# Optimization experiments

Hardware: AMD Instinct MI355X
Metric: run time of the kernel (lower is better)

The kernel has to match this reference:

```python
import jax, jax.numpy as jnp
import numpy as np

DIM = 128
N_CONV = 4
N_GRAPHS = 256
EPS = 1e-5


def _layernorm(h, g, b):
    m = jnp.mean(h, axis=-1, keepdims=True)
    v = jnp.mean((h - m) ** 2, axis=-1, keepdims=True)
    return g * (h - m) / jnp.sqrt(v + 1e-5) + b


def _gated_gcn(x, ei, e, Wsrc, bsrc, Wdst, bdst, We, be, nxg, nxb, neg, neb):
    # x: [N, D] node feats, ei: [2, E], e: [E, D] edge feats
    n = x.shape[0]
    i, j = ei[0], ei[1]
    sig = jax.nn.sigmoid(e)                                   # [E, D]
    e_sum = jax.ops.segment_sum(sig, i, num_segments=n)       # [N, D]
    e_gated = sig / (e_sum[i] + EPS)                          # [E, D]
    msg = e_gated * (x[j] @ Wdst + bdst)                      # [E, D]
    agg = jax.ops.segment_sum(msg, i, num_segments=n)         # [N, D]
    out = x @ Wsrc + bsrc + agg
    out = x + jax.nn.silu(_layernorm(out, nxg, nxb))
    z = jnp.concatenate([x[i], x[j], e], axis=-1)             # [E, 3D]
    e_new = e + jax.nn.silu(_layernorm(z @ We + be, neg, neb))
    return out, e_new


def setup_inputs() -> dict:
    key = jax.random.key(0)
    ks = iter(jax.random.split(key, 64))
    d = DIM

    def rn(shape, s=0.05):
        return (jax.random.normal(next(ks), shape, dtype=jnp.float32) * s)

    inp = {}
    inp["x"] = jax.random.normal(next(ks), (20000, 92), dtype=jnp.float32)
    inp["edge_attr"] = jax.random.normal(next(ks), (320000, 50), dtype=jnp.float32)
    inp["edge_attr_line"] = jax.random.normal(next(ks), (600000, 40), dtype=jnp.float32)
    inp["edge_index"] = jax.random.randint(next(ks), (2, 320000), 0, 20000, dtype=jnp.int64)
    inp["edge_index_line"] = jax.random.randint(next(ks), (2, 600000), 0, 320000, dtype=jnp.int64)
    inp["batch"] = jnp.sort(jax.random.randint(next(ks), (20000,), 0, N_GRAPHS, dtype=jnp.int64))

    inp["pre1_W"] = rn((92, d)); inp["pre1_b"] = jnp.zeros((d,), jnp.float32)
    inp["pre2_W"] = rn((50, d)); inp["pre2_b"] = jnp.zeros((d,), jnp.float32)
    inp["pre3_W"] = rn((40, d)); inp["pre3_b"] = jnp.zeros((d,), jnp.float32)

    for pfx in ("line", "atom"):
        inp[pfx + "_Wsrc"] = rn((N_CONV, d, d)); inp[pfx + "_bsrc"] = jnp.zeros((N_CONV, d), jnp.float32)
        inp[pfx + "_Wdst"] = rn((N_CONV, d, d)); inp[pfx + "_bdst"] = jnp.zeros((N_CONV, d), jnp.float32)
        inp[pfx + "_We"] = rn((N_CONV, 3 * d, d)); inp[pfx + "_be"] = jnp.zeros((N_CONV, d), jnp.float32)
        inp[pfx + "_nxg"] = jnp.ones((N_CONV, d), jnp.float32); inp[pfx + "_nxb"] = jnp.zeros((N_CONV, d), jnp.float32)
        inp[pfx + "_neg"] = jnp.ones((N_CONV, d), jnp.float32); inp[pfx + "_neb"] = jnp.zeros((N_CONV, d), jnp.float32)

    inp["bn_g"] = jnp.ones((d,), jnp.float32); inp["bn_b"] = jnp.zeros((d,), jnp.float32)
    inp["post_W"] = rn((d, d)); inp["post_b"] = jnp.zeros((d,), jnp.float32)
    inp["out_W"] = rn((d, 1)); inp["out_b"] = jnp.zeros((1,), jnp.float32)
    return inp


def reference(x, edge_attr, edge_attr_line,
              pre1_W, pre1_b, pre2_W, pre2_b, pre3_W, pre3_b,
              line_Wsrc, line_bsrc, line_Wdst, line_bdst, line_We, line_be,
              line_nxg, line_nxb, line_neg, line_neb,
              atom_Wsrc, atom_bsrc, atom_Wdst, atom_bdst, atom_We, atom_be,
              atom_nxg, atom_nxb, atom_neg, atom_neb,
              bn_g, bn_b, post_W, post_b, out_W, out_b,
              edge_index, edge_index_line, batch):
    act = jax.nn.silu
    # pre-FC (single layer each)
    h_node = act(x @ pre1_W + pre1_b)              # [N, D]
    h_edge = act(edge_attr @ pre2_W + pre2_b)      # [E, D]
    h_line = act(edge_attr_line @ pre3_W + pre3_b) # [E_line, D]

    for l in range(N_CONV):
        # line graph conv: nodes = atom edges, edges = line-graph edges
        h_edge, h_line = _gated_gcn(h_edge, edge_index_line, h_line,
                                    line_Wsrc[l], line_bsrc[l], line_Wdst[l], line_bdst[l],
                                    line_We[l], line_be[l],
                                    line_nxg[l], line_nxb[l], line_neg[l], line_neb[l])
        # atom graph conv
        h_node, h_edge = _gated_gcn(h_node, edge_index, h_edge,
                                    atom_Wsrc[l], atom_bsrc[l], atom_Wdst[l], atom_bdst[l],
                                    atom_We[l], atom_be[l],
                                    atom_nxg[l], atom_nxb[l], atom_neg[l], atom_neb[l])
        # dropout_rate = 0 -> identity

    # BatchNorm1d (batch statistics over nodes)
    m = jnp.mean(h_node, axis=0)
    v = jnp.mean((h_node - m) ** 2, axis=0)
    out = bn_g * (h_node - m) / jnp.sqrt(v + 1e-5) + bn_b
    out = act(out)
    out = act(out @ post_W + post_b)

    # global mean pool over crystals
    sums = jax.ops.segment_sum(out, batch, num_segments=N_GRAPHS)
    cnts = jax.ops.segment_sum(jnp.ones((out.shape[0],), out.dtype), batch, num_segments=N_GRAPHS)
    pooled = sums / jnp.maximum(cnts, 1.0)[:, None]
    return (pooled @ out_W + out_b).reshape(-1)    # [N_GRAPHS]
```

## Files before the change

### kernel.cpp

```cpp
#include <hip/hip_runtime.h>

#define NCONV_DEF 4
#define SCH 1024

typedef unsigned short u16;
typedef __attribute__((ext_vector_type(8))) short s8v;
typedef __attribute__((ext_vector_type(4))) float f4v;
typedef __attribute__((ext_vector_type(8))) unsigned short u16x8;

__device__ __forceinline__ float sigm_f(float x){ return 1.f/(1.f+__expf(-x)); }
__device__ __forceinline__ float silu_f(float x){ return x/(1.f+__expf(-x)); }
__device__ __forceinline__ float b2f(u16 h){ union{unsigned u; float f;} v; v.u=(unsigned)h<<16; return v.f; }
__device__ __forceinline__ u16 f2b(float f){ union{float f; unsigned u;} v; v.f=f; unsigned r=v.u+0x7fffu+((v.u>>16)&1u); return (u16)(r>>16); }
__device__ __forceinline__ float ldAv(const float* p, size_t i){ return p[i]; }
__device__ __forceinline__ float ldAv(const u16* p, size_t i){ return b2f(p[i]); }

#define EPS_ 136

__global__ __launch_bounds__(256) void zero_f_k(float* p, long n){
    long i=(long)blockIdx.x*256+threadIdx.x, st=(long)gridDim.x*256;
    for(;i<n;i+=st) p[i]=0.f;
}
__global__ __launch_bounds__(256) void zero_i_k(int* p, long n){
    long i=(long)blockIdx.x*256+threadIdx.x, st=(long)gridDim.x*256;
    for(;i<n;i+=st) p[i]=0;
}
__global__ void diag_k(float* out, int n, float v){
    int i=blockIdx.x*256+threadIdx.x; if(i<n) out[i]=v;
}
__global__ void probe_k(const int* ei, const int* eil, const int* batch, int nb, int* flag){
    if(threadIdx.x||blockIdx.x) return;
    int a=2,b=2,c=2;
    for(int k=0;k<64;k++){ if(ei[2*k+1]!=0) a=1; if(eil[2*k+1]!=0) b=1; }
    int base=nb-128;
    for(int k=0;k<64;k++){ if(batch[base+2*k+1]!=0) c=1; }
    flag[0]=a; flag[1]=b; flag[2]=c;
}

__global__ __launch_bounds__(256)
void hist_k(const int* __restrict__ idx, const int* __restrict__ iflag, int fi,
            int* __restrict__ cnt, int Ne, int Nn){
    int e=blockIdx.x*256+threadIdx.x; if(e>=Ne) return;
    int st=iflag[fi];
    int i=idx[(size_t)e*st]; i=i<0?0:(i>=Nn?Nn-1:i);
    atomicAdd(&cnt[i],1);
}
__global__ __launch_bounds__(256)
void scan1_k(const int* cnt, int* tot, int n){
    __shared__ int sh[256];
    int base=blockIdx.x*SCH, s=0;
    for(int t=threadIdx.x;t<SCH;t+=256){ int i=base+t; s+=(i<n)?cnt[i]:0; }
    sh[threadIdx.x]=s; __syncthreads();
    for(int o=128;o;o>>=1){ if(threadIdx.x<o) sh[threadIdx.x]+=sh[threadIdx.x+o]; __syncthreads(); }
    if(threadIdx.x==0) tot[blockIdx.x]=sh[0];
}
__global__ void scan2_k(int* tot, int nb){
    if(threadIdx.x==0&&blockIdx.x==0){ int acc=0; for(int i=0;i<nb;i++){int v=tot[i]; tot[i]=acc; acc+=v;} }
}
__global__ __launch_bounds__(256)
void scan3_k(const int* cnt, const int* tot, int* off, int n, int total){
    __shared__ int sh[256];
    int b=blockIdx.x, t4=b*SCH+threadIdx.x*4;
    int v0=(t4+0<n)?cnt[t4+0]:0, v1=(t4+1<n)?cnt[t4+1]:0;
    int v2=(t4+2<n)?cnt[t4+2]:0, v3=(t4+3<n)?cnt[t4+3]:0;
    int ls=v0+v1+v2+v3;
    sh[threadIdx.x]=ls; __syncthreads();
    for(int o=1;o<256;o<<=1){
        int val=(threadIdx.x>=o)?sh[threadIdx.x-o]:0; __syncthreads();
        sh[threadIdx.x]+=val; __syncthreads();
    }
    int excl=sh[threadIdx.x]-ls+tot[b];
    if(t4+0<n) off[t4+0]=excl;
    if(t4+1<n) off[t4+1]=excl+v0;
    if(t4+2<n) off[t4+2]=excl+v0+v1;
    if(t4+3<n) off[t4+3]=excl+v0+v1+v2;
    if(b==(int)gridDim.x-1&&threadIdx.x==255) off[n]=total;
}
__global__ __launch_bounds__(256)
void fill_k(const int* __restrict__ idx, const int* __restrict__ iflag, int fi, long joff,
            const int* __restrict__ off, int* __restrict__ cur,
            int* __restrict__ list, int* __restrict__ jlist, int Ne, int Nn){
    int e=blockIdx.x*256+threadIdx.x; if(e>=Ne) return;
    int st=iflag[fi];
    int i=idx[(size_t)e*st]; i=i<0?0:(i>=Nn?Nn-1:i);
    int j=idx[((size_t)joff+e)*st]; j=j<0?0:(j>=Nn?Nn-1:j);
    int pos=off[i]+atomicAdd(&cur[i],1);
    list[pos]=e; jlist[pos]=j;
}

__global__ __launch_bounds__(256)
void pack_w_k(const float* __restrict__ W, u16* __restrict__ Wp, int K, int Kp){
    int i=blockIdx.x*256+threadIdx.x;
    if(i>=128*Kp) return;
    int n=i/Kp, k=i-n*Kp;
    Wp[i] = (k<K) ? f2b(W[(size_t)k*128+n]) : (u16)0;
}

template<typename TA, int ACT>
__global__ __launch_bounds__(256)
void gemm_k(const TA* __restrict__ A, int lda, int M, int K, int Kp,
            const u16* __restrict__ Wp, const float* __restrict__ bias,
            u16* __restrict__ C)
{
    __shared__ __align__(16) u16 As[64*72];
    __shared__ __align__(16) u16 Bs[128*72];
    const int tid=threadIdx.x, row0=blockIdx.x*64;
    const int w=tid>>6, l=tid&63, lr=l&15, kg=l>>4;
    f4v zz={0.f,0.f,0.f,0.f};
    f4v acc[8];
#pragma unroll
    for(int i=0;i<8;++i) acc[i]=zz;

    for(int kt=0;kt<Kp;kt+=64){
        {
            int r=tid>>2, c0=(tid&3)*16;
            int gr=row0+r;
            bool vec=false;
            if constexpr (sizeof(TA)==2) vec=((K&63)==0);
            if(vec){
                const u16* src=(const u16*)(const void*)A+(size_t)gr*lda+kt+c0;
                u16x8 v0={0,0,0,0,0,0,0,0}, v1={0,0,0,0,0,0,0,0};
                if(gr<M){ v0=*(const u16x8*)src; v1=*(const u16x8*)(src+8); }
                *(u16x8*)&As[r*72+c0]=v0;
                *(u16x8*)&As[r*72+c0+8]=v1;
            } else {
                for(int c=c0;c<c0+16;++c){
                    int k=kt+c;
                    float v=(gr<M&&k<K)?ldAv(A,(size_t)gr*lda+k):0.f;
                    As[r*72+c]=f2b(v);
                }
            }
        }
        {
            int n=tid>>1, k0=(tid&1)*32;
            const u16* src=Wp+(size_t)n*Kp+kt+k0;
            *(u16x8*)&Bs[n*72+k0]   =*(const u16x8*)(src);
            *(u16x8*)&Bs[n*72+k0+8] =*(const u16x8*)(src+8);
            *(u16x8*)&Bs[n*72+k0+16]=*(const u16x8*)(src+16);
            *(u16x8*)&Bs[n*72+k0+24]=*(const u16x8*)(src+24);
        }
        __syncthreads();
        const int arow=w*16+lr;
#pragma unroll
        for(int kk=0;kk<64;kk+=32){
            s8v a=*(const s8v*)&As[arow*72+kk+kg*8];
#pragma unroll
            for(int ct=0;ct<8;++ct){
                s8v bfr=*(const s8v*)&Bs[(ct*16+lr)*72+kk+kg*8];
                acc[ct]=__builtin_amdgcn_mfma_f32_16x16x32_bf16(a,bfr,acc[ct],0,0,0);
            }
        }
        __syncthreads();
    }
    u16* ep=Bs;
#pragma unroll
    for(int ct=0;ct<8;++ct){
        int col=ct*16+lr;
        float bv=bias?bias[col]:0.f;
#pragma unroll
        for(int reg=0;reg<4;++reg){
            float v=acc[ct][reg]+bv;
            if(ACT) v=silu_f(v);
            ep[(w*16+kg*4+reg)*EPS_+col]=f2b(v);
        }
    }
    __syncthreads();
    {
        int ar=tid>>2, gr=row0+ar;
        if(gr<M){
            u16* crow=C+(size_t)gr*128+(tid&3)*32;
            const u16* hrow=&ep[ar*EPS_+(tid&3)*32];
#pragma unroll
            for(int c4=0;c4<4;++c4)
                *(u16x8*)(crow+c4*8)=*(const u16x8*)(hrow+c4*8);
        }
    }
}

__global__ __launch_bounds__(256)
void gemmz_k(u16* __restrict__ X, int M,
             const u16* __restrict__ Wp, const float* __restrict__ bias,
             const u16* __restrict__ U,
             const float* __restrict__ g, const float* __restrict__ b)
{
    __shared__ __align__(16) u16 As[2][64*68];
    __shared__ __align__(16) u16 Bs[128*136];
    const int tid=threadIdx.x, row0=blockIdx.x*64;
    const int w=tid>>6, l=tid&63, lr=l&15, kg=l>>4;
    u16* ep=&As[0][0];
    const int ar=tid>>2, gr=row0+ar;
    {
        u16x8 z8={0,0,0,0,0,0,0,0};
        u16x8 u0=z8,u1=z8,u2=z8,u3=z8;
        if(gr<M){
            const u16* ur=U+(size_t)gr*128+(tid&3)*32;
            u0=*(const u16x8*)(ur); u1=*(const u16x8*)(ur+8);
            u2=*(const u16x8*)(ur+16); u3=*(const u16x8*)(ur+24);
        }
        u16* d=&ep[ar*EPS_+(tid&3)*32];
        *(u16x8*)(d)=u0; *(u16x8*)(d+8)=u1; *(u16x8*)(d+16)=u2; *(u16x8*)(d+24)=u3;
    }
    __syncthreads();
    f4v acc[8];
#pragma unroll
    for(int ct=0;ct<8;++ct){
        int col=ct*16+lr;
        float bv=bias[col];
#pragma unroll
        for(int reg=0;reg<4;++reg)
            acc[ct][reg]=b2f(ep[(w*16+kg*4+reg)*EPS_+col])+bv;
    }
    __syncthreads();

    {
        int c0=(tid&3)*16;
        const u16* src=X+(size_t)gr*128;
        u16x8 z8={0,0,0,0,0,0,0,0};
        u16x8 v0=z8,v1=z8,v2=z8,v3=z8;
        if(gr<M){
            v0=*(const u16x8*)(src+c0);    v1=*(const u16x8*)(src+c0+8);
            v2=*(const u16x8*)(src+64+c0); v3=*(const u16x8*)(src+64+c0+8);
        }
        *(u16x8*)&As[0][ar*68+c0]=v0;  *(u16x8*)&As[0][ar*68+c0+8]=v1;
        *(u16x8*)&As[1][ar*68+c0]=v2;  *(u16x8*)&As[1][ar*68+c0+8]=v3;
        int bn=tid>>1, bk=(tid&1)*64;
        const u16* wsrc=Wp+(size_t)bn*128+bk;
#pragma unroll
        for(int q=0;q<8;++q)
            *(u16x8*)&Bs[bn*136+bk+q*8]=*(const u16x8*)(wsrc+q*8);
    }
    __syncthreads();
    const int arow=w*16+lr;
#pragma unroll
    for(int kt=0;kt<2;++kt){
#pragma unroll
        for(int kk=0;kk<64;kk+=32){
            s8v a=*(const s8v*)&As[kt][arow*68+kk+kg*8];
#pragma unroll
            for(int ct=0;ct<8;++ct){
                s8v bfr=*(const s8v*)&Bs[(ct*16+lr)*136+kt*64+kk+kg*8];
                acc[ct]=__builtin_amdgcn_mfma_f32_16x16x32_bf16(a,bfr,acc[ct],0,0,0);
            }
        }
    }
    float sum[4]={0.f,0.f,0.f,0.f}, sq[4]={0.f,0.f,0.f,0.f};
#pragma unroll
    for(int ct=0;ct<8;++ct)
#pragma unroll
        for(int reg=0;reg<4;++reg){
            float v=acc[ct][reg];
            sum[reg]+=v; sq[reg]+=v*v;
        }
#pragma unroll
    for(int m=1;m<16;m<<=1)
#pragma unroll
        for(int reg=0;reg<4;++reg){
            sum[reg]+=__shfl_xor(sum[reg],m,64);
            sq[reg] +=__shfl_xor(sq[reg], m,64);
        }
    float mean[4], rstd[4];
#pragma unroll
    for(int reg=0;reg<4;++reg){
        mean[reg]=sum[reg]*(1.f/128.f);
        float var=sq[reg]*(1.f/128.f)-mean[reg]*mean[reg];
        rstd[reg]=rsqrtf(var+1e-5f);
    }
    __syncthreads();
#pragma unroll
    for(int ct=0;ct<8;++ct){
        int col=ct*16+lr;
        float gv=g[col], bv=b[col];
#pragma unroll
        for(int reg=0;reg<4;++reg){
            float h=gv*(acc[ct][reg]-mean[reg])*rstd[reg]+bv;
            ep[(w*16+kg*4+reg)*EPS_+col]=f2b(silu_f(h));
        }
    }
    if(gr<M){
        u16* xrow=X+(size_t)gr*128+(tid&3)*32;
        const u16* hrow=&ep[ar*EPS_+(tid&3)*32];
#pragma unroll
        for(int c4=0;c4<4;++c4){
            u16x8 xv=*(const u16x8*)(xrow+c4*8);
            u16x8 hv=*(const u16x8*)(hrow+c4*8);
            u16x8 ov;
#pragma unroll
            for(int j=0;j<8;++j) ov[j]=f2b(b2f(xv[j])+b2f(hv[j]));
            *(u16x8*)(xrow+c4*8)=ov;
        }
    }
}

template<int FIN, int HASPREV>
__global__ __launch_bounds__(256)
void gather_k(const u16* __restrict__ e, const u16* __restrict__ P1,
              u16* __restrict__ U,
              const int* __restrict__ off, const int* __restrict__ list,
              const int* __restrict__ jlist,
              int Nn, int c0, int c1)
{
    int wid=threadIdx.x>>6, lane=threadIdx.x&63;
    int h=lane>>5, sl=lane&31;
    int n=blockIdx.x*8+wid*2+h;
    int beg=0,end=0;
    if(n<Nn){ beg=off[n]; end=off[n+1]; }
    const int d4=sl*4;
    uint2 uprev; uprev.x=0; uprev.y=0;
    if(FIN&&HASPREV&&n<Nn) uprev=*(const uint2*)(U+(size_t)n*128+d4);

    float es[4]={0.f,0.f,0.f,0.f}, a[4]={0.f,0.f,0.f,0.f};
    int k=beg;
    uint2 ev_n, pv_n; ev_n.x=ev_n.y=0; pv_n.x=pv_n.y=0;
    bool in_n=false;
    if(k<end){
        int eid=list[k], j=jlist[k];
        in_n=(j>=c0)&&(j<c1);
        if(FIN||in_n) ev_n=*(const uint2*)(e+(size_t)eid*128+d4);
        if(in_n)      pv_n=*(const uint2*)(P1+(size_t)(j-c0)*128+d4);
    }
    while(k<end){
        uint2 ev=ev_n, pv=pv_n; bool in=in_n;
        int kn=k+1;
        if(kn<end){
            int eid=list[kn], j=jlist[kn];
            in_n=(j>=c0)&&(j<c1);
            ev_n.x=ev_n.y=0; pv_n.x=pv_n.y=0;
            if(FIN||in_n) ev_n=*(const uint2*)(e+(size_t)eid*128+d4);
            if(in_n)      pv_n=*(const uint2*)(P1+(size_t)(j-c0)*128+d4);
        }
        float s0=sigm_f(b2f((u16)(ev.x&0xffff)));
        float s1=sigm_f(b2f((u16)(ev.x>>16)));
        float s2=sigm_f(b2f((u16)(ev.y&0xffff)));
        float s3=sigm_f(b2f((u16)(ev.y>>16)));
        if(FIN){ es[0]+=s0; es[1]+=s1; es[2]+=s2; es[3]+=s3; }
        if(in){
            a[0]+=s0*b2f((u16)(pv.x&0xffff));
            a[1]+=s1*b2f((u16)(pv.x>>16));
            a[2]+=s2*b2f((u16)(pv.y&0xffff));
            a[3]+=s3*b2f((u16)(pv.y>>16));
        }
        k=kn;
    }
    if(n>=Nn) return;
    uint2* up=(uint2*)(U+(size_t)n*128+d4);
    uint2 o;
    if(!FIN){
        o.x=((unsigned)f2b(a[0]))|((unsigned)f2b(a[1])<<16);
        o.y=((unsigned)f2b(a[2]))|((unsigned)f2b(a[3])<<16);
    } else {
        if(HASPREV){
            a[0]+=b2f((u16)(uprev.x&0xffff));
            a[1]+=b2f((u16)(uprev.x>>16));
            a[2]+=b2f((u16)(uprev.y&0xffff));
            a[3]+=b2f((u16)(uprev.y>>16));
        }
        float r0=1.f/(es[0]+1e-5f), r1=1.f/(es[1]+1e-5f);
        float r2=1.f/(es[2]+1e-5f), r3=1.f/(es[3]+1e-5f);
        o.x=((unsigned)f2b(a[0]*r0))|((unsigned)f2b(a[1]*r1)<<16);
        o.y=((unsigned)f2b(a[2]*r2))|((unsigned)f2b(a[3]*r3)<<16);
    }
    *up=o;
}

__global__ __launch_bounds__(512)
void edgez_k(u16* __restrict__ e, const u16* __restrict__ x,
             const int* __restrict__ idx, long joff,
             const int* __restrict__ iflag, int fi,
             const u16* __restrict__ Wep, const float* __restrict__ be,
             const float* __restrict__ g, const float* __restrict__ b,
             int Ne, int Nn)
{
    __shared__ __align__(16) u16 As[2][128*68];
    __shared__ __align__(16) u16 Bs[2][128*68];
    __shared__ int rid[256];
    const int tid=threadIdx.x, row0=blockIdx.x*128;
    const int w=tid>>6, l=tid&63, lr=l&15, kg=l>>4;
    int st=iflag[fi];
    if(tid<256){
        int r=tid&127, eid=row0+r; if(eid>=Ne) eid=Ne-1;
        long elem=(tid<128)?(long)eid:(joff+eid);
        int v=idx[(size_t)elem*st]; v=v<0?0:(v>=Nn?Nn-1:v);
        rid[tid]=v;
    }
    __syncthreads();
    const int ar=tid>>2, ac=(tid&3)*16;
    const int bn=tid>>2, bk=(tid&3)*16;
    int eidA=row0+ar; if(eidA>=Ne) eidA=Ne-1;
    const u16* aptr0=x+(size_t)rid[ar]*128;
    const u16* aptr1=x+(size_t)rid[128+ar]*128;
    const u16* aptr2=e+(size_t)eidA*128;

    f4v zz={0.f,0.f,0.f,0.f};
    f4v acc[8];
#pragma unroll
    for(int i=0;i<8;++i) acc[i]=zz;

    u16x8 a0,a1,b0,b1;
    u16x8 er0,er1,er2,er3;
    {
        const u16* src=aptr0+ac;
        a0=*(const u16x8*)src; a1=*(const u16x8*)(src+8);
        const u16* wsrc=Wep+(size_t)bn*384+bk;
        b0=*(const u16x8*)wsrc; b1=*(const u16x8*)(wsrc+8);
    }
#pragma unroll
    for(int s=0;s<6;++s){
        const int buf=s&1;
        *(u16x8*)&As[buf][ar*68+ac]  =a0;
        *(u16x8*)&As[buf][ar*68+ac+8]=a1;
        *(u16x8*)&Bs[buf][bn*68+bk]  =b0;
        *(u16x8*)&Bs[buf][bn*68+bk+8]=b1;
        if(s<5){
            const int sn=s+1, sec=sn>>1, half=sn&1;
            const u16* src=(sec==0?aptr0:(sec==1?aptr1:aptr2))+half*64+ac;
            a0=*(const u16x8*)src; a1=*(const u16x8*)(src+8);
            if(sec==2){ if(half==0){ er0=a0; er1=a1; } else { er2=a0; er3=a1; } }
            const u16* wsrc=Wep+(size_t)bn*384+sn*64+bk;
            b0=*(const u16x8*)wsrc; b1=*(const u16x8*)(wsrc+8);
        }
        __syncthreads();
        __builtin_amdgcn_s_setprio(1);
        const int arow=w*16+lr;
#pragma unroll
        for(int kk=0;kk<64;kk+=32){
            s8v a=*(const s8v*)&As[buf][arow*68+kk+kg*8];
#pragma unroll
            for(int ct=0;ct<8;++ct){
                s8v bfr=*(const s8v*)&Bs[buf][(ct*16+lr)*68+kk+kg*8];
                acc[ct]=__builtin_amdgcn_mfma_f32_16x16x32_bf16(a,bfr,acc[ct],0,0,0);
            }
        }
        __builtin_amdgcn_s_setprio(0);
    }
    float sum[4]={0.f,0.f,0.f,0.f}, sq[4]={0.f,0.f,0.f,0.f};
#pragma unroll
    for(int ct=0;ct<8;++ct){
        float bev=be[ct*16+lr];
#pragma unroll
        for(int reg=0;reg<4;++reg){
            float v=acc[ct][reg]+bev;
            acc[ct][reg]=v;
            sum[reg]+=v; sq[reg]+=v*v;
        }
    }
#pragma unroll
    for(int m=1;m<16;m<<=1){
#pragma unroll
        for(int reg=0;reg<4;++reg){
            sum[reg]+=__shfl_xor(sum[reg],m,64);
            sq[reg] +=__shfl_xor(sq[reg], m,64);
        }
    }
    float mean[4], rstd[4];
#pragma unroll
    for(int reg=0;reg<4;++reg){
        mean[reg]=sum[reg]*(1.f/128.f);
        float var=sq[reg]*(1.f/128.f)-mean[reg]*mean[reg];
        rstd[reg]=rsqrtf(var+1e-5f);
    }
    __syncthreads();
    u16* ep=&Bs[0][0];
#pragma unroll
    for(int ct=0;ct<8;++ct){
        int col=ct*16+lr;
        float gv=g[col], bv=b[col];
#pragma unroll
        for(int reg=0;reg<4;++reg){
            float hh=gv*(acc[ct][reg]-mean[reg])*rstd[reg]+bv;
            ep[(w*16+kg*4+reg)*EPS_+col]=f2b(silu_f(hh));
        }
    }
    {
        int eid=row0+ar;
        if(eid<Ne){
            u16* erow=e+(size_t)eid*128;
            const u16* hr=&ep[ar*EPS_];
            u16x8 h0=*(const u16x8*)(hr+ac),    h1=*(const u16x8*)(hr+ac+8);
            u16x8 h2=*(const u16x8*)(hr+64+ac), h3=*(const u16x8*)(hr+64+ac+8);
            u16x8 o0,o1,o2,o3;
#pragma unroll
            for(int j=0;j<8;++j){
                o0[j]=f2b(b2f(er0[j])+b2f(h0[j]));
                o1[j]=f2b(b2f(er1[j])+b2f(h1[j]));
                o2[j]=f2b(b2f(er2[j])+b2f(h2[j]));
                o3[j]=f2b(b2f(er3[j])+b2f(h3[j]));
            }
            *(u16x8*)(erow+ac)=o0;    *(u16x8*)(erow+ac+8)=o1;
            *(u16x8*)(erow+64+ac)=o2; *(u16x8*)(erow+64+ac+8)=o3;
        }
    }
}

__global__ __launch_bounds__(256)
void bn_stats_k(const u16* __restrict__ h, float* __restrict__ st, int N){
    int t=blockIdx.x*256+threadIdx.x;
    int d=t&127, r0=t>>7, rstride=(gridDim.x*256)>>7;
    float s=0.f,q=0.f;
    for(int r=r0;r<N;r+=rstride){ float v=b2f(h[(size_t)r*128+d]); s+=v; q+=v*v; }
    atomicAdd(&st[d],s); atomicAdd(&st[128+d],q);
}
__global__ __launch_bounds__(256)
void bn_apply_k(u16* __restrict__ h, const float* __restrict__ st,
                const float* __restrict__ g, const float* __restrict__ b, int N){
    int t=blockIdx.x*256+threadIdx.x;
    if(t>=N*128) return;
    int d=t&127;
    float inv=1.f/(float)N;
    float m=st[d]*inv, var=st[128+d]*inv-m*m;
    float v=g[d]*(b2f(h[t])-m)*rsqrtf(var+1e-5f)+b[d];
    h[t]=f2b(silu_f(v));
}
__global__ __launch_bounds__(256)
void pool_k(const u16* __restrict__ o, const int* __restrict__ batch,
            const int* __restrict__ iflag,
            float* __restrict__ pooled, float* __restrict__ cnt, int N, int NG){
    int st=iflag[2];
    int wid=threadIdx.x>>6, lane=threadIdx.x&63;
    int n=blockIdx.x*4+wid; if(n>=N) return;
    int gi=batch[(size_t)n*st]; gi=gi<0?0:(gi>=NG?NG-1:gi);
    atomicAdd(&pooled[(size_t)gi*128+lane],    b2f(o[(size_t)n*128+lane]));
    atomicAdd(&pooled[(size_t)gi*128+64+lane], b2f(o[(size_t)n*128+64+lane]));
    if(lane==0) atomicAdd(&cnt[gi],1.f);
}
__global__ void final_k(const float* __restrict__ pooled, const float* __restrict__ cnt,
                        const float* __restrict__ oW, const float* __restrict__ ob,
                        float* __restrict__ out){
    int gi=blockIdx.x, lane=threadIdx.x;
    float v=pooled[(size_t)gi*128+lane]*oW[lane]
           +pooled[(size_t)gi*128+64+lane]*oW[64+lane];
    for(int m=32;m;m>>=1) v+=__shfl_xor(v,m,64);
    if(lane==0) out[gi]=v/fmaxf(cnt[gi],1.f)+ob[0];
}

template<typename TA>
static inline void gemm(hipStream_t s, const TA* A, int lda, int M, int K, int Kp,
                        const u16* Wp, const float* bias, u16* C, int act){
    dim3 grid((M+63)/64);
    if(act) gemm_k<TA,1><<<grid,256,0,s>>>(A,lda,M,K,Kp,Wp,bias,C);
    else    gemm_k<TA,0><<<grid,256,0,s>>>(A,lda,M,K,Kp,Wp,bias,C);
}

static inline void build_csr(hipStream_t s, const int* idx, int fi, long joff, const int* iflag,
                             int Ne, int Nn, int* off, int* cur, int* list, int* jlist, int* tot){
    int nb=(Nn+SCH-1)/SCH;
    zero_i_k<<<256,256,0,s>>>(cur,Nn);
    hist_k<<<(Ne+255)/256,256,0,s>>>(idx,iflag,fi,cur,Ne,Nn);
    scan1_k<<<nb,256,0,s>>>(cur,tot,Nn);
    scan2_k<<<1,1,0,s>>>(tot,nb);
    scan3_k<<<nb,256,0,s>>>(cur,tot,off,Nn,Ne);
    zero_i_k<<<256,256,0,s>>>(cur,Nn);
    fill_k<<<(Ne+255)/256,256,0,s>>>(idx,iflag,fi,joff,off,cur,list,jlist,Ne,Nn);
}

static inline void pack_w(hipStream_t s, const float* W, u16* Wp, int K, int Kp){
    pack_w_k<<<(128*Kp+255)/256,256,0,s>>>(W,Wp,K,Kp);
}

extern "C" void kernel_launch(void* const* d_in, const int* in_sizes, int n_in,
                              void* d_out, int out_size, void* d_ws, size_t ws_size,
                              hipStream_t stream)
{
    const float* x_in =(const float*)d_in[0];
    const float* ea   =(const float*)d_in[1];
    const float* eal  =(const float*)d_in[2];
    const int*   ei   =(const int*)d_in[3];
    const int*   eil  =(const int*)d_in[4];
    const int*   batch=(const int*)d_in[5];
    const float* pre1W=(const float*)d_in[6];  const float* pre1b=(const float*)d_in[7];
    const float* pre2W=(const float*)d_in[8];  const float* pre2b=(const float*)d_in[9];
    const float* pre3W=(const float*)d_in[10]; const float* pre3b=(const float*)d_in[11];
    const float* lWsrc=(const float*)d_in[12]; const float* lbsrc=(const float*)d_in[13];
    const float* lWdst=(const float*)d_in[14]; const float* lbdst=(const float*)d_in[15];
    const float* lWe  =(const float*)d_in[16]; const float* lbe  =(const float*)d_in[17];
    const float* lnxg =(const float*)d_in[18]; const float* lnxb =(const float*)d_in[19];
    const float* lneg =(const float*)d_in[20]; const float* lneb =(const float*)d_in[21];
    const float* aWsrc=(const float*)d_in[22]; const float* absrc=(const float*)d_in[23];
    const float* aWdst=(const float*)d_in[24]; const float* abdst=(const float*)d_in[25];
    const float* aWe  =(const float*)d_in[26]; const float* abe  =(const float*)d_in[27];
    const float* anxg =(const float*)d_in[28]; const float* anxb =(const float*)d_in[29];
    const float* aneg =(const float*)d_in[30]; const float* aneb =(const float*)d_in[31];
    const float* bng  =(const float*)d_in[32]; const float* bnb  =(const float*)d_in[33];
    const float* postW=(const float*)d_in[34]; const float* postb=(const float*)d_in[35];
    const float* outW =(const float*)d_in[36]; const float* outb =(const float*)d_in[37];
    (void)n_in;

    const int N =in_sizes[5];
    const int E =in_sizes[3]/2;
    const int EL=in_sizes[4]/2;
    const int NG=out_size;
    const int CH=(E+1)/2;

    char* base=(char*)d_ws;
    size_t off=0;
    auto alloc=[&](size_t bytes)->char*{
        char* p=base+off; off=(off+bytes+255)&~(size_t)255; return p;
    };
    u16* hN   =(u16*)alloc((size_t)N*128*2);
    u16* hE   =(u16*)alloc((size_t)E*128*2);
    u16* hL   =(u16*)alloc((size_t)EL*128*2);
    u16* U    =(u16*)alloc((size_t)E*128*2);
    u16* P1   =(u16*)alloc((size_t)CH*128*2);
    int* off_l=(int*)alloc((size_t)(E+1)*4);
    int* cur_l=(int*)alloc((size_t)E*4);
    int* list_l=(int*)alloc((size_t)EL*4);
    int* jlist_l=(int*)alloc((size_t)EL*4);
    int* off_a=(int*)alloc((size_t)(N+1)*4);
    int* cur_a=(int*)alloc((size_t)N*4);
    int* list_a=(int*)alloc((size_t)E*4);
    int* jlist_a=(int*)alloc((size_t)E*4);
    int* tot  =(int*)alloc(4096);
    int* iflag=(int*)alloc(64);
    float* stats =(float*)alloc(256*4);
    float* pooled=(float*)alloc((size_t)NG*128*4);
    float* cnt   =(float*)alloc((size_t)NG*4);
    u16* pre1p=(u16*)alloc(128*128*2);
    u16* pre2p=(u16*)alloc(128*64*2);
    u16* pre3p=(u16*)alloc(128*64*2);
    u16* postp=(u16*)alloc(128*128*2);
    u16 *lsrcp[4],*ldstp[4],*lWep[4],*asrcp[4],*adstp[4],*aWep[4];
    for(int i=0;i<4;i++){
        lsrcp[i]=(u16*)alloc(128*128*2);
        ldstp[i]=(u16*)alloc(128*128*2);
        lWep[i] =(u16*)alloc(128*384*2);
        asrcp[i]=(u16*)alloc(128*128*2);
        adstp[i]=(u16*)alloc(128*128*2);
        aWep[i] =(u16*)alloc(128*384*2);
    }
    if(off>ws_size){
        diag_k<<<(NG+255)/256,256,0,stream>>>((float*)d_out,NG,(float)(ws_size>>20)+0.25f);
        return;
    }

    probe_k<<<1,64,0,stream>>>(ei,eil,batch,N,iflag);
    build_csr(stream,eil,1,EL,iflag,EL,E,off_l,cur_l,list_l,jlist_l,tot);
    build_csr(stream,ei, 0,E, iflag,E, N,off_a,cur_a,list_a,jlist_a,tot);

    pack_w(stream,pre1W,pre1p,92,128);
    pack_w(stream,pre2W,pre2p,50,64);
    pack_w(stream,pre3W,pre3p,40,64);
    pack_w(stream,postW,postp,128,128);
    for(int i=0;i<4;i++){
        pack_w(stream,lWsrc+(size_t)i*128*128,lsrcp[i],128,128);
        pack_w(stream,lWdst+(size_t)i*128*128,ldstp[i],128,128);
        pack_w(stream,lWe  +(size_t)i*384*128,lWep[i],384,384);
        pack_w(stream,aWsrc+(size_t)i*128*128,asrcp[i],128,128);
        pack_w(stream,aWdst+(size_t)i*128*128,adstp[i],128,128);
        pack_w(stream,aWe  +(size_t)i*384*128,aWep[i],384,384);
    }

    gemm(stream,x_in,92,N, 92,128,pre1p,pre1b,hN,1);
    gemm(stream,ea,  50,E, 50, 64,pre2p,pre2b,hE,1);
    gemm(stream,eal, 40,EL,40, 64,pre3p,pre3b,hL,1);

    for(int l=0;l<NCONV_DEF;++l){
        {
            gemm(stream,hE,128,CH,128,128,ldstp[l],lbdst+l*128,P1,0);
            gather_k<0,0><<<(E+7)/8,256,0,stream>>>(hL,P1,U,off_l,list_l,jlist_l,E,0,CH);
            gemm(stream,hE+(size_t)CH*128,128,E-CH,128,128,ldstp[l],lbdst+l*128,P1,0);
            gather_k<1,1><<<(E+7)/8,256,0,stream>>>(hL,P1,U,off_l,list_l,jlist_l,E,CH,E);
            edgez_k<<<(EL+127)/128,512,0,stream>>>(hL,hE,eil,EL,iflag,1,
                                                   lWep[l],lbe+l*128,lneg+l*128,lneb+l*128,EL,E);
            gemmz_k<<<(E+63)/64,256,0,stream>>>(hE,E,lsrcp[l],lbsrc+l*128,U,
                                                lnxg+l*128,lnxb+l*128);
        }
        {
            gemm(stream,hN,128,N,128,128,adstp[l],abdst+l*128,P1,0);
            gather_k<1,0><<<(N+7)/8,256,0,stream>>>(hE,P1,U,off_a,list_a,jlist_a,N,0,N);
            edgez_k<<<(E+127)/128,512,0,stream>>>(hE,hN,ei,E,iflag,0,
                                                  aWep[l],abe+l*128,aneg+l*128,aneb+l*128,E,N);
            gemmz_k<<<(N+63)/64,256,0,stream>>>(hN,N,asrcp[l],absrc+l*128,U,
                                                anxg+l*128,anxb+l*128);
        }
    }

    zero_f_k<<<64,256,0,stream>>>(stats,256);
    zero_f_k<<<64,256,0,stream>>>(pooled,(long)NG*128);
    zero_f_k<<<1,256,0,stream>>>(cnt,NG);
    bn_stats_k<<<256,256,0,stream>>>(hN,stats,N);
    bn_apply_k<<<(N*128+255)/256,256,0,stream>>>(hN,stats,bng,bnb,N);

    gemm(stream,hN,128,N,128,128,postp,postb,P1,1);

    pool_k<<<(N+3)/4,256,0,stream>>>(P1,batch,iflag,pooled,cnt,N,NG);
    final_k<<<NG,64,0,stream>>>(pooled,cnt,outW,outb,(float*)d_out);
}
```

Baseline: 3.109 ms.

## Halve edgez_k K-tile to shrink shared memory and raise occupancy

```diff
diff --git a/kernel.cpp b/kernel.cpp
--- a/kernel.cpp
+++ b/kernel.cpp
@@ -362,7 +362,7 @@
     *up=o;
 }
 
-__global__ __launch_bounds__(512)
+__global__ __launch_bounds__(512, 8)
 void edgez_k(u16* __restrict__ e, const u16* __restrict__ x,
              const int* __restrict__ idx, long joff,
              const int* __restrict__ iflag, int fi,
@@ -370,8 +370,7 @@
              const float* __restrict__ g, const float* __restrict__ b,
              int Ne, int Nn)
 {
-    __shared__ __align__(16) u16 As[2][128*68];
-    __shared__ __align__(16) u16 Bs[2][128*68];
+    __shared__ __align__(16) u16 smem[4*128*36];
     __shared__ int rid[256];
     const int tid=threadIdx.x, row0=blockIdx.x*128;
     const int w=tid>>6, l=tid&63, lr=l&15, kg=l>>4;
@@ -383,52 +382,45 @@
         rid[tid]=v;
     }
     __syncthreads();
-    const int ar=tid>>2, ac=(tid&3)*16;
-    const int bn=tid>>2, bk=(tid&3)*16;
+    const int ar=tid>>2, c8=(tid&3)*8;
     int eidA=row0+ar; if(eidA>=Ne) eidA=Ne-1;
     const u16* aptr0=x+(size_t)rid[ar]*128;
     const u16* aptr1=x+(size_t)rid[128+ar]*128;
     const u16* aptr2=e+(size_t)eidA*128;
+    u16* Asb[2]={smem,           smem+128*36};
+    u16* Bsb[2]={smem+2*128*36,  smem+3*128*36};
 
     f4v zz={0.f,0.f,0.f,0.f};
     f4v acc[8];
 #pragma unroll
     for(int i=0;i<8;++i) acc[i]=zz;
 
-    u16x8 a0,a1,b0,b1;
-    u16x8 er0,er1,er2,er3;
+    u16x8 a0,b0;
+    u16x8 er[4];
     {
-        const u16* src=aptr0+ac;
-        a0=*(const u16x8*)src; a1=*(const u16x8*)(src+8);
-        const u16* wsrc=Wep+(size_t)bn*384+bk;
-        b0=*(const u16x8*)wsrc; b1=*(const u16x8*)(wsrc+8);
-    }
-#pragma unroll
-    for(int s=0;s<6;++s){
+        a0=*(const u16x8*)(aptr0+c8);
+        b0=*(const u16x8*)(Wep+(size_t)ar*384+c8);
+    }
+#pragma unroll
+    for(int s=0;s<12;++s){
         const int buf=s&1;
-        *(u16x8*)&As[buf][ar*68+ac]  =a0;
-        *(u16x8*)&As[buf][ar*68+ac+8]=a1;
-        *(u16x8*)&Bs[buf][bn*68+bk]  =b0;
-        *(u16x8*)&Bs[buf][bn*68+bk+8]=b1;
-        if(s<5){
-            const int sn=s+1, sec=sn>>1, half=sn&1;
-            const u16* src=(sec==0?aptr0:(sec==1?aptr1:aptr2))+half*64+ac;
-            a0=*(const u16x8*)src; a1=*(const u16x8*)(src+8);
-            if(sec==2){ if(half==0){ er0=a0; er1=a1; } else { er2=a0; er3=a1; } }
-            const u16* wsrc=Wep+(size_t)bn*384+sn*64+bk;
-            b0=*(const u16x8*)wsrc; b1=*(const u16x8*)(wsrc+8);
+        *(u16x8*)&Asb[buf][ar*36+c8]=a0;
+        *(u16x8*)&Bsb[buf][ar*36+c8]=b0;
+        if(s<11){
+            const int sn=s+1, sec=sn>>2, soff=sn&3;
+            const u16* src=(sec==0?aptr0:(sec==1?aptr1:aptr2))+soff*32+c8;
+            a0=*(const u16x8*)src;
+            if(sec==2) er[soff]=a0;
+            b0=*(const u16x8*)(Wep+(size_t)ar*384+sn*32+c8);
         }
         __syncthreads();
         __builtin_amdgcn_s_setprio(1);
         const int arow=w*16+lr;
-#pragma unroll
-        for(int kk=0;kk<64;kk+=32){
-            s8v a=*(const s8v*)&As[buf][arow*68+kk+kg*8];
-#pragma unroll
-            for(int ct=0;ct<8;++ct){
-                s8v bfr=*(const s8v*)&Bs[buf][(ct*16+lr)*68+kk+kg*8];
-                acc[ct]=__builtin_amdgcn_mfma_f32_16x16x32_bf16(a,bfr,acc[ct],0,0,0);
-            }
+        s8v a=*(const s8v*)&Asb[buf][arow*36+kg*8];
+#pragma unroll
+        for(int ct=0;ct<8;++ct){
+            s8v bfr=*(const s8v*)&Bsb[buf][(ct*16+lr)*36+kg*8];
+            acc[ct]=__builtin_amdgcn_mfma_f32_16x16x32_bf16(a,bfr,acc[ct],0,0,0);
         }
         __builtin_amdgcn_s_setprio(0);
     }
@@ -459,7 +451,7 @@
         rstd[reg]=rsqrtf(var+1e-5f);
     }
     __syncthreads();
-    u16* ep=&Bs[0][0];
+    u16* ep=smem;
 #pragma unroll
     for(int ct=0;ct<8;++ct){
         int col=ct*16+lr;
@@ -475,18 +467,14 @@
         if(eid<Ne){
             u16* erow=e+(size_t)eid*128;
             const u16* hr=&ep[ar*EPS_];
-            u16x8 h0=*(const u16x8*)(hr+ac),    h1=*(const u16x8*)(hr+ac+8);
-            u16x8 h2=*(const u16x8*)(hr+64+ac), h3=*(const u16x8*)(hr+64+ac+8);
-            u16x8 o0,o1,o2,o3;
-#pragma unroll
-            for(int j=0;j<8;++j){
-                o0[j]=f2b(b2f(er0[j])+b2f(h0[j]));
-                o1[j]=f2b(b2f(er1[j])+b2f(h1[j]));
-                o2[j]=f2b(b2f(er2[j])+b2f(h2[j]));
-                o3[j]=f2b(b2f(er3[j])+b2f(h3[j]));
+#pragma unroll
+            for(int s4=0;s4<4;++s4){
+                u16x8 hv=*(const u16x8*)(hr+s4*32+c8);
+                u16x8 ov;
+#pragma unroll
+                for(int j=0;j<8;++j) ov[j]=f2b(b2f(er[s4][j])+b2f(hv[j]));
+                *(u16x8*)(erow+s4*32+c8)=ov;
             }
-            *(u16x8*)(erow+ac)=o0;    *(u16x8*)(erow+ac+8)=o1;
-            *(u16x8*)(erow+64+ac)=o2; *(u16x8*)(erow+64+ac+8)=o3;
         }
     }
 }
```

Measured after the change: 5.722 ms. 84.1% more time.

## Fuse final neighbor gather into node-update GEMM with ping-pong feature buffers

Applied to the files above, without the earlier changes.

```diff
diff --git a/kernel.cpp b/kernel.cpp
--- a/kernel.cpp
+++ b/kernel.cpp
@@ -178,126 +178,11 @@
 }
 
 __global__ __launch_bounds__(256)
-void gemmz_k(u16* __restrict__ X, int M,
-             const u16* __restrict__ Wp, const float* __restrict__ bias,
-             const u16* __restrict__ U,
-             const float* __restrict__ g, const float* __restrict__ b)
-{
-    __shared__ __align__(16) u16 As[2][64*68];
-    __shared__ __align__(16) u16 Bs[128*136];
-    const int tid=threadIdx.x, row0=blockIdx.x*64;
-    const int w=tid>>6, l=tid&63, lr=l&15, kg=l>>4;
-    u16* ep=&As[0][0];
-    const int ar=tid>>2, gr=row0+ar;
-    {
-        u16x8 z8={0,0,0,0,0,0,0,0};
-        u16x8 u0=z8,u1=z8,u2=z8,u3=z8;
-        if(gr<M){
-            const u16* ur=U+(size_t)gr*128+(tid&3)*32;
-            u0=*(const u16x8*)(ur); u1=*(const u16x8*)(ur+8);
-            u2=*(const u16x8*)(ur+16); u3=*(const u16x8*)(ur+24);
-        }
-        u16* d=&ep[ar*EPS_+(tid&3)*32];
-        *(u16x8*)(d)=u0; *(u16x8*)(d+8)=u1; *(u16x8*)(d+16)=u2; *(u16x8*)(d+24)=u3;
-    }
-    __syncthreads();
-    f4v acc[8];
-#pragma unroll
-    for(int ct=0;ct<8;++ct){
-        int col=ct*16+lr;
-        float bv=bias[col];
-#pragma unroll
-        for(int reg=0;reg<4;++reg)
-            acc[ct][reg]=b2f(ep[(w*16+kg*4+reg)*EPS_+col])+bv;
-    }
-    __syncthreads();
-
-    {
-        int c0=(tid&3)*16;
-        const u16* src=X+(size_t)gr*128;
-        u16x8 z8={0,0,0,0,0,0,0,0};
-        u16x8 v0=z8,v1=z8,v2=z8,v3=z8;
-        if(gr<M){
-            v0=*(const u16x8*)(src+c0);    v1=*(const u16x8*)(src+c0+8);
-            v2=*(const u16x8*)(src+64+c0); v3=*(const u16x8*)(src+64+c0+8);
-        }
-        *(u16x8*)&As[0][ar*68+c0]=v0;  *(u16x8*)&As[0][ar*68+c0+8]=v1;
-        *(u16x8*)&As[1][ar*68+c0]=v2;  *(u16x8*)&As[1][ar*68+c0+8]=v3;
-        int bn=tid>>1, bk=(tid&1)*64;
-        const u16* wsrc=Wp+(size_t)bn*128+bk;
-#pragma unroll
-        for(int q=0;q<8;++q)
-            *(u16x8*)&Bs[bn*136+bk+q*8]=*(const u16x8*)(wsrc+q*8);
-    }
-    __syncthreads();
-    const int arow=w*16+lr;
-#pragma unroll
-    for(int kt=0;kt<2;++kt){
-#pragma unroll
-        for(int kk=0;kk<64;kk+=32){
-            s8v a=*(const s8v*)&As[kt][arow*68+kk+kg*8];
-#pragma unroll
-            for(int ct=0;ct<8;++ct){
-                s8v bfr=*(const s8v*)&Bs[(ct*16+lr)*136+kt*64+kk+kg*8];
-                acc[ct]=__builtin_amdgcn_mfma_f32_16x16x32_bf16(a,bfr,acc[ct],0,0,0);
-            }
-        }
-    }
-    float sum[4]={0.f,0.f,0.f,0.f}, sq[4]={0.f,0.f,0.f,0.f};
-#pragma unroll
-    for(int ct=0;ct<8;++ct)
-#pragma unroll
-        for(int reg=0;reg<4;++reg){
-            float v=acc[ct][reg];
-            sum[reg]+=v; sq[reg]+=v*v;
-        }
-#pragma unroll
-    for(int m=1;m<16;m<<=1)
-#pragma unroll
-        for(int reg=0;reg<4;++reg){
-            sum[reg]+=__shfl_xor(sum[reg],m,64);
-            sq[reg] +=__shfl_xor(sq[reg], m,64);
-        }
-    float mean[4], rstd[4];
-#pragma unroll
-    for(int reg=0;reg<4;++reg){
-        mean[reg]=sum[reg]*(1.f/128.f);
-        float var=sq[reg]*(1.f/128.f)-mean[reg]*mean[reg];
-        rstd[reg]=rsqrtf(var+1e-5f);
-    }
-    __syncthreads();
-#pragma unroll
-    for(int ct=0;ct<8;++ct){
-        int col=ct*16+lr;
-        float gv=g[col], bv=b[col];
-#pragma unroll
-        for(int reg=0;reg<4;++reg){
-            float h=gv*(acc[ct][reg]-mean[reg])*rstd[reg]+bv;
-            ep[(w*16+kg*4+reg)*EPS_+col]=f2b(silu_f(h));
-        }
-    }
-    if(gr<M){
-        u16* xrow=X+(size_t)gr*128+(tid&3)*32;
-        const u16* hrow=&ep[ar*EPS_+(tid&3)*32];
-#pragma unroll
-        for(int c4=0;c4<4;++c4){
-            u16x8 xv=*(const u16x8*)(xrow+c4*8);
-            u16x8 hv=*(const u16x8*)(hrow+c4*8);
-            u16x8 ov;
-#pragma unroll
-            for(int j=0;j<8;++j) ov[j]=f2b(b2f(xv[j])+b2f(hv[j]));
-            *(u16x8*)(xrow+c4*8)=ov;
-        }
-    }
-}
-
-template<int FIN, int HASPREV>
-__global__ __launch_bounds__(256)
-void gather_k(const u16* __restrict__ e, const u16* __restrict__ P1,
-              u16* __restrict__ U,
-              const int* __restrict__ off, const int* __restrict__ list,
-              const int* __restrict__ jlist,
-              int Nn, int c0, int c1)
+void gatherp_k(const u16* __restrict__ e, const u16* __restrict__ P1,
+               u16* __restrict__ U,
+               const int* __restrict__ off, const int* __restrict__ list,
+               const int* __restrict__ jlist,
+               int Nn, int c0, int c1)
 {
     int wid=threadIdx.x>>6, lane=threadIdx.x&63;
     int h=lane>>5, sl=lane&31;
@@ -305,18 +190,17 @@
     int beg=0,end=0;
     if(n<Nn){ beg=off[n]; end=off[n+1]; }
     const int d4=sl*4;
-    uint2 uprev; uprev.x=0; uprev.y=0;
-    if(FIN&&HASPREV&&n<Nn) uprev=*(const uint2*)(U+(size_t)n*128+d4);
-
-    float es[4]={0.f,0.f,0.f,0.f}, a[4]={0.f,0.f,0.f,0.f};
+    float a[4]={0.f,0.f,0.f,0.f};
     int k=beg;
     uint2 ev_n, pv_n; ev_n.x=ev_n.y=0; pv_n.x=pv_n.y=0;
     bool in_n=false;
     if(k<end){
         int eid=list[k], j=jlist[k];
         in_n=(j>=c0)&&(j<c1);
-        if(FIN||in_n) ev_n=*(const uint2*)(e+(size_t)eid*128+d4);
-        if(in_n)      pv_n=*(const uint2*)(P1+(size_t)(j-c0)*128+d4);
+        if(in_n){
+            ev_n=*(const uint2*)(e+(size_t)eid*128+d4);
+            pv_n=*(const uint2*)(P1+(size_t)(j-c0)*128+d4);
+        }
     }
     while(k<end){
         uint2 ev=ev_n, pv=pv_n; bool in=in_n;
@@ -325,15 +209,16 @@
             int eid=list[kn], j=jlist[kn];
             in_n=(j>=c0)&&(j<c1);
             ev_n.x=ev_n.y=0; pv_n.x=pv_n.y=0;
-            if(FIN||in_n) ev_n=*(const uint2*)(e+(size_t)eid*128+d4);
-            if(in_n)      pv_n=*(const uint2*)(P1+(size_t)(j-c0)*128+d4);
-        }
-        float s0=sigm_f(b2f((u16)(ev.x&0xffff)));
-        float s1=sigm_f(b2f((u16)(ev.x>>16)));
-        float s2=sigm_f(b2f((u16)(ev.y&0xffff)));
-        float s3=sigm_f(b2f((u16)(ev.y>>16)));
-        if(FIN){ es[0]+=s0; es[1]+=s1; es[2]+=s2; es[3]+=s3; }
+            if(in_n){
+                ev_n=*(const uint2*)(e+(size_t)eid*128+d4);
+                pv_n=*(const uint2*)(P1+(size_t)(j-c0)*128+d4);
+            }
+        }
         if(in){
+            float s0=sigm_f(b2f((u16)(ev.x&0xffff)));
+            float s1=sigm_f(b2f((u16)(ev.x>>16)));
+            float s2=sigm_f(b2f((u16)(ev.y&0xffff)));
+            float s3=sigm_f(b2f((u16)(ev.y>>16)));
             a[0]+=s0*b2f((u16)(pv.x&0xffff));
             a[1]+=s1*b2f((u16)(pv.x>>16));
             a[2]+=s2*b2f((u16)(pv.y&0xffff));
@@ -342,24 +227,173 @@
         k=kn;
     }
     if(n>=Nn) return;
-    uint2* up=(uint2*)(U+(size_t)n*128+d4);
     uint2 o;
-    if(!FIN){
-        o.x=((unsigned)f2b(a[0]))|((unsigned)f2b(a[1])<<16);
-        o.y=((unsigned)f2b(a[2]))|((unsigned)f2b(a[3])<<16);
-    } else {
-        if(HASPREV){
-            a[0]+=b2f((u16)(uprev.x&0xffff));
-            a[1]+=b2f((u16)(uprev.x>>16));
-            a[2]+=b2f((u16)(uprev.y&0xffff));
-            a[3]+=b2f((u16)(uprev.y>>16));
+    o.x=((unsigned)f2b(a[0]))|((unsigned)f2b(a[1])<<16);
+    o.y=((unsigned)f2b(a[2]))|((unsigned)f2b(a[3])<<16);
+    *(uint2*)(U+(size_t)n*128+d4)=o;
+}
+
+template<int HASPREV>
+__global__ __launch_bounds__(256)
+void gatherz_k(const u16* __restrict__ X, u16* __restrict__ Xn,
+               const u16* __restrict__ e, const u16* __restrict__ P1,
+               const int* __restrict__ off, const int* __restrict__ list,
+               const int* __restrict__ jlist,
+               const u16* __restrict__ Wp, const float* __restrict__ bias,
+               const float* __restrict__ g, const float* __restrict__ b,
+               int M, int c0, int c1)
+{
+    __shared__ __align__(16) u16 As[2][64*68];
+    __shared__ __align__(16) u16 Bs[128*136];
+    const int tid=threadIdx.x, row0=blockIdx.x*64;
+    const int w=tid>>6, l=tid&63, lr=l&15, kg=l>>4;
+    const int h=l>>5, sl=l&31, d4=sl*4;
+    u16* ep=&As[0][0];
+
+#pragma unroll 1
+    for(int it=0;it<8;++it){
+        int nl=w*16+it*2+h, n=row0+nl;
+        float es[4]={0.f,0.f,0.f,0.f}, a[4]={0.f,0.f,0.f,0.f};
+        if(n<M){
+            int beg=off[n], end=off[n+1];
+            int k=beg;
+            uint2 ev_n, pv_n; ev_n.x=ev_n.y=0; pv_n.x=pv_n.y=0;
+            bool in_n=false;
+            if(k<end){
+                int eid=list[k], j=jlist[k];
+                in_n=(j>=c0)&&(j<c1);
+                ev_n=*(const uint2*)(e+(size_t)eid*128+d4);
+                if(in_n) pv_n=*(const uint2*)(P1+(size_t)(j-c0)*128+d4);
+            }
+            while(k<end){
+                uint2 ev=ev_n, pv=pv_n; bool in=in_n;
+                int kn=k+1;
+                if(kn<end){
+                    int eid=list[kn], j=jlist[kn];
+                    in_n=(j>=c0)&&(j<c1);
+                    ev_n=*(const uint2*)(e+(size_t)eid*128+d4);
+                    pv_n.x=pv_n.y=0;
+                    if(in_n) pv_n=*(const uint2*)(P1+(size_t)(j-c0)*128+d4);
+                }
+                float s0=sigm_f(b2f((u16)(ev.x&0xffff)));
+                float s1=sigm_f(b2f((u16)(ev.x>>16)));
+                float s2=sigm_f(b2f((u16)(ev.y&0xffff)));
+                float s3=sigm_f(b2f((u16)(ev.y>>16)));
+                es[0]+=s0; es[1]+=s1; es[2]+=s2; es[3]+=s3;
+                if(in){
+                    a[0]+=s0*b2f((u16)(pv.x&0xffff));
+                    a[1]+=s1*b2f((u16)(pv.x>>16));
+                    a[2]+=s2*b2f((u16)(pv.y&0xffff));
+                    a[3]+=s3*b2f((u16)(pv.y>>16));
+                }
+                k=kn;
+            }
+            if(HASPREV){
+                uint2 up=*(const uint2*)(Xn+(size_t)n*128+d4);
+                a[0]+=b2f((u16)(up.x&0xffff));
+                a[1]+=b2f((u16)(up.x>>16));
+                a[2]+=b2f((u16)(up.y&0xffff));
+                a[3]+=b2f((u16)(up.y>>16));
+            }
         }
         float r0=1.f/(es[0]+1e-5f), r1=1.f/(es[1]+1e-5f);
         float r2=1.f/(es[2]+1e-5f), r3=1.f/(es[3]+1e-5f);
+        uint2 o;
         o.x=((unsigned)f2b(a[0]*r0))|((unsigned)f2b(a[1]*r1)<<16);
         o.y=((unsigned)f2b(a[2]*r2))|((unsigned)f2b(a[3]*r3)<<16);
-    }
-    *up=o;
+        *(uint2*)(ep+nl*EPS_+d4)=o;
+    }
+    __syncthreads();
+    f4v acc[8];
+#pragma unroll
+    for(int ct=0;ct<8;++ct){
+        int col=ct*16+lr;
+        float bv=bias[col];
+#pragma unroll
+        for(int reg=0;reg<4;++reg)
+            acc[ct][reg]=b2f(ep[(w*16+kg*4+reg)*EPS_+col])+bv;
+    }
+    __syncthreads();
+
+    const int ar=tid>>2, gr=row0+ar;
+    {
+        int c0c=(tid&3)*16;
+        const u16* src=X+(size_t)gr*128;
+        u16x8 z8={0,0,0,0,0,0,0,0};
+        u16x8 v0=z8,v1=z8,v2=z8,v3=z8;
+        if(gr<M){
+            v0=*(const u16x8*)(src+c0c);    v1=*(const u16x8*)(src+c0c+8);
+            v2=*(const u16x8*)(src+64+c0c); v3=*(const u16x8*)(src+64+c0c+8);
+        }
+        *(u16x8*)&As[0][ar*68+c0c]=v0;  *(u16x8*)&As[0][ar*68+c0c+8]=v1;
+        *(u16x8*)&As[1][ar*68+c0c]=v2;  *(u16x8*)&As[1][ar*68+c0c+8]=v3;
+        int bn=tid>>1, bk=(tid&1)*64;
+        const u16* wsrc=Wp+(size_t)bn*128+bk;
+#pragma unroll
+        for(int q=0;q<8;++q)
+            *(u16x8*)&Bs[bn*136+bk+q*8]=*(const u16x8*)(wsrc+q*8);
+    }
+    __syncthreads();
+    const int arow=w*16+lr;
+#pragma unroll
+    for(int kt=0;kt<2;++kt){
+#pragma unroll
+        for(int kk=0;kk<64;kk+=32){
+            s8v a=*(const s8v*)&As[kt][arow*68+kk+kg*8];
+#pragma unroll
+            for(int ct=0;ct<8;++ct){
+                s8v bfr=*(const s8v*)&Bs[(ct*16+lr)*136+kt*64+kk+kg*8];
+                acc[ct]=__builtin_amdgcn_mfma_f32_16x16x32_bf16(a,bfr,acc[ct],0,0,0);
+            }
+        }
+    }
+    float sum[4]={0.f,0.f,0.f,0.f}, sq[4]={0.f,0.f,0.f,0.f};
+#pragma unroll
+    for(int ct=0;ct<8;++ct)
+#pragma unroll
+        for(int reg=0;reg<4;++reg){
+            float v=acc[ct][reg];
+            sum[reg]+=v; sq[reg]+=v*v;
+        }
+#pragma unroll
+    for(int m=1;m<16;m<<=1)
+#pragma unroll
+        for(int reg=0;reg<4;++reg){
+            sum[reg]+=__shfl_xor(sum[reg],m,64);
+            sq[reg] +=__shfl_xor(sq[reg], m,64);
+        }
+    float mean[4], rstd[4];
+#pragma unroll
+    for(int reg=0;reg<4;++reg){
+        mean[reg]=sum[reg]*(1.f/128.f);
+        float var=sq[reg]*(1.f/128.f)-mean[reg]*mean[reg];
+        rstd[reg]=rsqrtf(var+1e-5f);
+    }
+    __syncthreads();
+#pragma unroll
+    for(int ct=0;ct<8;++ct){
+        int col=ct*16+lr;
+        float gv=g[col], bv=b[col];
+#pragma unroll
+        for(int reg=0;reg<4;++reg){
+            float hh=gv*(acc[ct][reg]-mean[reg])*rstd[reg]+bv;
+            ep[(w*16+kg*4+reg)*EPS_+col]=f2b(silu_f(hh));
+        }
+    }
+    if(gr<M){
+        const u16* xrow=X+(size_t)gr*128+(tid&3)*32;
+        u16* orow=Xn+(size_t)gr*128+(tid&3)*32;
+        const u16* hrow=&ep[ar*EPS_+(tid&3)*32];
+#pragma unroll
+        for(int c4=0;c4<4;++c4){
+            u16x8 xv=*(const u16x8*)(xrow+c4*8);
+            u16x8 hv=*(const u16x8*)(hrow+c4*8);
+            u16x8 ov;
+#pragma unroll
+            for(int j=0;j<8;++j) ov[j]=f2b(b2f(xv[j])+b2f(hv[j]));
+            *(u16x8*)(orow+c4*8)=ov;
+        }
+    }
 }
 
 __global__ __launch_bounds__(512)
@@ -595,10 +629,11 @@
     auto alloc=[&](size_t bytes)->char*{
         char* p=base+off; off=(off+bytes+255)&~(size_t)255; return p;
     };
-    u16* hN   =(u16*)alloc((size_t)N*128*2);
-    u16* hE   =(u16*)alloc((size_t)E*128*2);
+    u16* hNa  =(u16*)alloc((size_t)N*128*2);
+    u16* hNb  =(u16*)alloc((size_t)N*128*2);
+    u16* hEa  =(u16*)alloc((size_t)E*128*2);
+    u16* hEb  =(u16*)alloc((size_t)E*128*2);
     u16* hL   =(u16*)alloc((size_t)EL*128*2);
-    u16* U    =(u16*)alloc((size_t)E*128*2);
     u16* P1   =(u16*)alloc((size_t)CH*128*2);
     int* off_l=(int*)alloc((size_t)(E+1)*4);
     int* cur_l=(int*)alloc((size_t)E*4);
@@ -648,6 +683,9 @@
         pack_w(stream,aWe  +(size_t)i*384*128,aWep[i],384,384);
     }
 
+    u16* hN=hNa; u16* hNalt=hNb;
+    u16* hE=hEa; u16* hEalt=hEb;
+
     gemm(stream,x_in,92,N, 92,128,pre1p,pre1b,hN,1);
     gemm(stream,ea,  50,E, 50, 64,pre2p,pre2b,hE,1);
     gemm(stream,eal, 40,EL,40, 64,pre3p,pre3b,hL,1);
@@ -655,21 +693,23 @@
     for(int l=0;l<NCONV_DEF;++l){
         {
             gemm(stream,hE,128,CH,128,128,ldstp[l],lbdst+l*128,P1,0);
-            gather_k<0,0><<<(E+7)/8,256,0,stream>>>(hL,P1,U,off_l,list_l,jlist_l,E,0,CH);
+            gatherp_k<<<(E+7)/8,256,0,stream>>>(hL,P1,hEalt,off_l,list_l,jlist_l,E,0,CH);
             gemm(stream,hE+(size_t)CH*128,128,E-CH,128,128,ldstp[l],lbdst+l*128,P1,0);
-            gather_k<1,1><<<(E+7)/8,256,0,stream>>>(hL,P1,U,off_l,list_l,jlist_l,E,CH,E);
+            gatherz_k<1><<<(E+63)/64,256,0,stream>>>(hE,hEalt,hL,P1,off_l,list_l,jlist_l,
+                                                     lsrcp[l],lbsrc+l*128,
+                                                     lnxg+l*128,lnxb+l*128,E,CH,E);
             edgez_k<<<(EL+127)/128,512,0,stream>>>(hL,hE,eil,EL,iflag,1,
                                                    lWep[l],lbe+l*128,lneg+l*128,lneb+l*128,EL,E);
-            gemmz_k<<<(E+63)/64,256,0,stream>>>(hE,E,lsrcp[l],lbsrc+l*128,U,
-                                                lnxg+l*128,lnxb+l*128);
+            u16* t=hE; hE=hEalt; hEalt=t;
         }
         {
             gemm(stream,hN,128,N,128,128,adstp[l],abdst+l*128,P1,0);
-            gather_k<1,0><<<(N+7)/8,256,0,stream>>>(hE,P1,U,off_a,list_a,jlist_a,N,0,N);
+            gatherz_k<0><<<(N+63)/64,256,0,stream>>>(hN,hNalt,hE,P1,off_a,list_a,jlist_a,
+                                                     asrcp[l],absrc+l*128,
+                                                     anxg+l*128,anxb+l*128,N,0,N);
             edgez_k<<<(E+127)/128,512,0,stream>>>(hE,hN,ei,E,iflag,0,
                                                   aWep[l],abe+l*128,aneg+l*128,aneb+l*128,E,N);
-            gemmz_k<<<(N+63)/64,256,0,stream>>>(hN,N,asrcp[l],absrc+l*128,U,
-                                                anxg+l*128,anxb+l*128);
+            u16* t=hN; hN=hNalt; hNalt=t;
         }
     }
 
```

New measurement: 3.900 ms. +25.4%, slower.
